# Kernel optimization log

Measured on AMD Instinct MI355X. Metric: run time of the kernel, lower is better.

## Reference

```python
import jax, jax.numpy as jnp
import numpy as np

N_LAYERS, H, D, DFF, V = 6, 16, 1024, 4096, 512
B, S = 4, 2048
DK = D // H
EPS = 1e-6
NEG = -1000000000.0


def _pe_table(max_len, d):
    pos = np.arange(max_len, dtype=np.float32)[:, None]
    div = 1.0 / (10000.0 ** (np.arange(0, d, 2, dtype=np.float32) / d))
    pe = np.zeros((max_len, d), dtype=np.float32)
    pe[:, 0::2] = np.sin(pos * div)
    pe[:, 1::2] = np.cos(pos * div)
    return jnp.asarray(pe[None])  # [1, max_len, d]


def setup_inputs() -> dict:
    key = jax.random.key(0)
    ks = jax.random.split(key, 20)
    f = lambda k, shp: (jax.random.normal(k, shp, dtype=jnp.float32) * 0.02)
    inp = {
        "tgt": jax.random.randint(ks[0], (B, S), 0, V, dtype=jnp.int64),
        "tgt_mask": jnp.tril(jnp.ones((S, S), dtype=jnp.int32))[None],  # [1,S,S] causal
        "emb": f(ks[1], (V, D)),
        "pe": _pe_table(S, D),
        "Wq": f(ks[2], (N_LAYERS, H, D, DK)), "bq": f(ks[3], (N_LAYERS, H, DK)),
        "Wk": f(ks[4], (N_LAYERS, H, D, DK)), "bk": f(ks[5], (N_LAYERS, H, DK)),
        "Wv": f(ks[6], (N_LAYERS, H, D, DK)), "bv": f(ks[7], (N_LAYERS, H, DK)),
        "Wo": f(ks[8], (N_LAYERS, D, D)), "bo": f(ks[9], (N_LAYERS, D)),
        "W1": f(ks[10], (N_LAYERS, D, DFF)), "b1": f(ks[11], (N_LAYERS, DFF)),
        "W2": f(ks[12], (N_LAYERS, DFF, D)), "b2": f(ks[13], (N_LAYERS, D)),
        "ln1_a": jnp.ones((N_LAYERS, D)), "ln1_b": jnp.zeros((N_LAYERS, D)),
        "ln2_a": jnp.ones((N_LAYERS, D)), "ln2_b": jnp.zeros((N_LAYERS, D)),
        "lnf_a": jnp.ones((D,)), "lnf_b": jnp.zeros((D,)),
    }
    return inp


def _ln(x, a, b):
    # torch: a*(x-mean)/(std+eps)+b with unbiased std
    m = x.mean(-1, keepdims=True)
    var = ((x - m) ** 2).sum(-1, keepdims=True) / (x.shape[-1] - 1)
    return a * (x - m) / (jnp.sqrt(var) + EPS) + b


def reference(tgt, tgt_mask, emb, pe, Wq, bq, Wk, bk, Wv, bv, Wo, bo,
              W1, b1, W2, b2, ln1_a, ln1_b, ln2_a, ln2_b, lnf_a, lnf_b):
    d = emb.shape[1]
    s = tgt.shape[1]
    x = emb[tgt] * jnp.sqrt(jnp.float32(d)) + pe[:, :s]  # [B,S,D]
    dk = Wq.shape[-1]
    scale = jnp.sqrt(jnp.float32(dk))

    def layer(x, p):
        wq, bq_, wk, bk_, wv, bv_, wo, bo_, w1, b1_, w2, b2_, a1, g1, a2, g2 = p
        h = _ln(x, a1, g1)
        q = jnp.einsum('bsd,hdk->bhsk', h, wq) + bq_[:, None, :]
        k = jnp.einsum('bsd,hdk->bhsk', h, wk) + bk_[:, None, :]
        v = jnp.einsum('bsd,hdk->bhsk', h, wv) + bv_[:, None, :]
        sc = jnp.einsum('bhsk,bhtk->bhst', q, k) / scale
        sc = jnp.where(tgt_mask[:, None] == 0, jnp.float32(NEG), sc)
        att = jax.nn.softmax(sc, axis=-1)
        o = jnp.einsum('bhst,bhtk->bhsk', att, v)
        o = o.transpose(0, 2, 1, 3).reshape(x.shape)  # concat heads (head order)
        x = x + (o @ wo + bo_)
        h2 = _ln(x, a2, g2)
        x = x + (jnp.maximum(h2 @ w1 + b1_, 0.0) @ w2 + b2_)
        return x, None

    x, _ = jax.lax.scan(layer, x, (Wq, bq, Wk, bk, Wv, bv, Wo, bo,
                                   W1, b1, W2, b2, ln1_a, ln1_b, ln2_a, ln2_b))
    return _ln(x, lnf_a, lnf_b)
```

## Files before the change

kernel.cpp:

```cpp
#include <hip/hip_runtime.h>

typedef __bf16 bf16;
typedef float f32x4 __attribute__((ext_vector_type(4)));
typedef __bf16 bf16x8 __attribute__((ext_vector_type(8)));
typedef __bf16 bf16x4 __attribute__((ext_vector_type(4)));
typedef __bf16 bf16x2 __attribute__((ext_vector_type(2)));

#define NL 6
#define NH 16
#define DM 1024
#define DFF 4096
#define SEQ 2048
#define NB 4
#define NTOK (NB*SEQ)

__device__ __forceinline__ void gload16(const void* g, void* l) {
  __builtin_amdgcn_global_load_lds((const __attribute__((address_space(1))) void*)g,
                                   (__attribute__((address_space(3))) void*)l, 16, 0, 0);
}

__global__ __launch_bounds__(256) void repack_t(const float* __restrict__ src,
                                                bf16* __restrict__ out, int K, int N) {
  const int l = blockIdx.z;
  const int d0 = blockIdx.x * 32, n0 = blockIdx.y * 32;
  __shared__ float t[32][33];
  const int tx = threadIdx.x & 31, ty = threadIdx.x >> 5;
  const float* s = src + (size_t)l * K * N;
  #pragma unroll
  for (int j = 0; j < 4; ++j)
    t[ty*4 + j][tx] = s[(size_t)(d0 + ty*4 + j) * N + n0 + tx];
  __syncthreads();
  bf16* o = out + (size_t)l * N * K;
  #pragma unroll
  for (int j = 0; j < 4; ++j)
    o[(size_t)(n0 + ty*4 + j) * K + d0 + tx] = (bf16)t[tx][ty*4 + j];
}

__global__ __launch_bounds__(256) void repack_qkv(const float* __restrict__ Wq,
                                                  const float* __restrict__ Wk,
                                                  const float* __restrict__ Wv,
                                                  bf16* __restrict__ out) {
  const int l = blockIdx.z;
  const int d0 = blockIdx.x * 32, n0 = blockIdx.y * 32;
  __shared__ float t[32][33];
  const int tx = threadIdx.x & 31, ty = threadIdx.x >> 5;
  const int which = n0 >> 10, h = (n0 & 1023) >> 6, kh0 = n0 & 63;
  const float* W = (which == 0) ? Wq : (which == 1 ? Wk : Wv);
  const float* s = W + ((size_t)(l*NH + h) * DM) * 64 + kh0;
  #pragma unroll
  for (int j = 0; j < 4; ++j)
    t[ty*4 + j][tx] = s[(size_t)(d0 + ty*4 + j) * 64 + tx];
  __syncthreads();
  bf16* o = out + (size_t)l * 3072 * DM + (size_t)n0 * DM + d0;
  #pragma unroll
  for (int j = 0; j < 4; ++j)
    o[(size_t)(ty*4 + j) * DM + tx] = (bf16)t[tx][ty*4 + j];
}

__global__ __launch_bounds__(256) void repack_b(const float* __restrict__ bq,
                                                const float* __restrict__ bk,
                                                const float* __restrict__ bv,
                                                float* __restrict__ out) {
  const int i = blockIdx.x * 256 + threadIdx.x;
  if (i >= NL * 3072) return;
  const int l = i / 3072, n = i % 3072;
  const int which = n >> 10, h = (n >> 6) & 15, kh = n & 63;
  const float* b = (which == 0) ? bq : (which == 1 ? bk : bv);
  out[i] = b[(l*NH + h) * 64 + kh];
}

__global__ __launch_bounds__(256) void embed_k(const int* __restrict__ tgt,
                                               const float* __restrict__ emb,
                                               const float* __restrict__ pe,
                                               float* __restrict__ x) {
  const int i = blockIdx.x;
  const int spos = i & (SEQ - 1);
  const int tok = tgt[i];
  const int tid = threadIdx.x;
  float4 e = ((const float4*)(emb + (size_t)tok * DM))[tid];
  float4 p = ((const float4*)(pe + (size_t)spos * DM))[tid];
  float4 r; r.x = e.x*32.f + p.x; r.y = e.y*32.f + p.y; r.z = e.z*32.f + p.z; r.w = e.w*32.f + p.w;
  ((float4*)(x + (size_t)i * DM))[tid] = r;
}

template<bool OB>
__global__ __launch_bounds__(256) void ln_k(const float* __restrict__ x,
                                            const float* __restrict__ a,
                                            const float* __restrict__ bsh,
                                            bf16* __restrict__ ob, float* __restrict__ of) {
  __shared__ float red[8];
  const int row = blockIdx.x, tid = threadIdx.x;
  const float4 v = ((const float4*)(x + (size_t)row * DM))[tid];
  float s = v.x + v.y + v.z + v.w;
  #pragma unroll
  for (int off = 32; off > 0; off >>= 1) s += __shfl_down(s, off);
  if ((tid & 63) == 0) red[tid >> 6] = s;
  __syncthreads();
  const float mean = (red[0] + red[1] + red[2] + red[3]) * (1.f / 1024.f);
  const float d0 = v.x - mean, d1 = v.y - mean, d2 = v.z - mean, d3 = v.w - mean;
  float ss = d0*d0 + d1*d1 + d2*d2 + d3*d3;
  #pragma unroll
  for (int off = 32; off > 0; off >>= 1) ss += __shfl_down(ss, off);
  if ((tid & 63) == 0) red[4 + (tid >> 6)] = ss;
  __syncthreads();
  const float var = (red[4] + red[5] + red[6] + red[7]) * (1.f / 1023.f);
  const float inv = 1.f / (sqrtf(var) + 1e-6f);
  const float4 av = ((const float4*)a)[tid];
  const float4 bv = ((const float4*)bsh)[tid];
  const float r0 = av.x * d0 * inv + bv.x;
  const float r1 = av.y * d1 * inv + bv.y;
  const float r2 = av.z * d2 * inv + bv.z;
  const float r3 = av.w * d3 * inv + bv.w;
  if (OB) {
    bf16x4 w; w[0] = (bf16)r0; w[1] = (bf16)r1; w[2] = (bf16)r2; w[3] = (bf16)r3;
    ((bf16x4*)(ob + (size_t)row * DM))[tid] = w;
  } else {
    float4 w; w.x = r0; w.y = r1; w.z = r2; w.w = r3;
    ((float4*)(of + (size_t)row * DM))[tid] = w;
  }
}

#define BARRIER() asm volatile("s_barrier" ::: "memory")
#define VMW(n)    asm volatile("s_waitcnt vmcnt(" #n ")" ::: "memory")

template<int EPI>
__global__ __launch_bounds__(512, 1) void gemm8(const bf16* __restrict__ A,
                                                const bf16* __restrict__ B,
                                                const float* __restrict__ bias,
                                                float* __restrict__ xres,
                                                bf16* __restrict__ outb,
                                                bf16* __restrict__ vtb,
                                                int K, int ldc) {
  constexpr bool SW = (EPI == 1) || (EPI == 2);
  __shared__ __align__(16) char lds[131072];
  const int tid = threadIdx.x;
  const int m0 = blockIdx.x * 256, n0 = blockIdx.y * 256;
  const int wid = tid >> 6, lane = tid & 63;
  const int wm = wid >> 2, wn = wid & 3;
  const int fr = lane & 15, fq = lane >> 4;
  const int fl16 = (fq * 16 + fr) * 16;
  const int s0 = tid, s1 = tid + 512;
  const int r0 = ((s0 >> 7) << 4) | (s0 & 15), c0 = (((s0 >> 6) & 1) << 2) | ((s0 >> 4) & 3);
  const int r1 = ((s1 >> 7) << 4) | (s1 & 15), c1 = (((s1 >> 6) & 1) << 2) | ((s1 >> 4) & 3);
  const bf16* Ap0 = A + (size_t)(m0 + r0) * K + c0 * 8;
  const bf16* Ap1 = A + (size_t)(m0 + r1) * K + c1 * 8;
  const bf16* Bp0 = B + (size_t)(n0 + r0) * K + c0 * 8;
  const bf16* Bp1 = B + (size_t)(n0 + r1) * K + c1 * 8;
  const size_t rskip = (size_t)128 * K;
  const int aRd = wm * 16384;
  const int bRd = 32768 + (wn >> 1) * 16384;
  const int bN = (wn & 1) * 4;

  f32x4 acc[8][4] = {};
  bf16x8 af8[8][2], bfr[4][2];

#define ST_A(d, h, kt) { \
  gload16(Ap0 + (size_t)(h) * rskip + (kt), lds + (d)*65536 + (h)*16384 + s0*16); \
  gload16(Ap1 + (size_t)(h) * rskip + (kt), lds + (d)*65536 + (h)*16384 + s1*16); }
#define ST_B(d, h, kt) { \
  gload16(Bp0 + (size_t)(h) * rskip + (kt), lds + (d)*65536 + 32768 + (h)*16384 + s0*16); \
  gload16(Bp1 + (size_t)(h) * rskip + (kt), lds + (d)*65536 + 32768 + (h)*16384 + s1*16); }
#define LD_A(d, mb) { _Pragma("unroll") for (int m_ = 0; m_ < 4; ++m_) \
    _Pragma("unroll") for (int ks_ = 0; ks_ < 2; ++ks_) \
      af8[(mb) + m_][ks_] = *(const bf16x8*)(lds + (d)*65536 + aRd + ((mb) + m_)*2048 + ks_*1024 + fl16); }
#define LD_B(d, nb) { _Pragma("unroll") for (int n_ = 0; n_ < 2; ++n_) \
    _Pragma("unroll") for (int ks_ = 0; ks_ < 2; ++ks_) \
      bfr[(nb) + n_][ks_] = *(const bf16x8*)(lds + (d)*65536 + bRd + (bN + (nb) + n_)*2048 + ks_*1024 + fl16); }
#define MFMA_Q(mb, nb) { __builtin_amdgcn_s_setprio(1); \
  _Pragma("unroll") for (int m_ = 0; m_ < 4; ++m_) \
  _Pragma("unroll") for (int n_ = 0; n_ < 2; ++n_) \
  _Pragma("unroll") for (int ks_ = 0; ks_ < 2; ++ks_) \
    acc[(mb) + m_][(nb) + n_] = SW ? \
      __builtin_amdgcn_mfma_f32_16x16x32_bf16( \
        bfr[(nb) + n_][ks_], af8[(mb) + m_][ks_], acc[(mb) + m_][(nb) + n_], 0, 0, 0) : \
      __builtin_amdgcn_mfma_f32_16x16x32_bf16( \
        af8[(mb) + m_][ks_], bfr[(nb) + n_][ks_], acc[(mb) + m_][(nb) + n_], 0, 0, 0); \
  __builtin_amdgcn_s_setprio(0); }

  ST_A(0, 0, 0); ST_A(0, 1, 0);
  ST_B(0, 0, 0); ST_B(0, 1, 0);
  ST_A(1, 0, 64); ST_A(1, 1, 64);
  VMW(4);
  BARRIER();

  const int niter = K >> 7;
  for (int it = 0; it < niter; ++it) {
    const int ktB1 = (2 * it + 1) << 6;
    const int ktE2 = (2 * it + 2) << 6;
    const int ktO3 = (2 * it + 3) << 6;
    const bool more = (it + 1 < niter);
    LD_A(0, 0); LD_B(0, 0);
    ST_B(1, 0, ktB1);
    BARRIER(); MFMA_Q(0, 0); BARRIER();
    LD_A(0, 4);
    ST_B(1, 1, ktB1);
    BARRIER(); MFMA_Q(4, 0); BARRIER();
    LD_B(0, 2);
    if (more) ST_A(0, 0, ktE2);
    BARRIER(); MFMA_Q(4, 2); BARRIER();
    if (more) { ST_A(0, 1, ktE2); VMW(4); } else { VMW(0); }
    BARRIER(); MFMA_Q(0, 2); BARRIER();
    LD_A(1, 0); LD_B(1, 0);
    if (more) ST_B(0, 0, ktE2);
    BARRIER(); MFMA_Q(0, 0); BARRIER();
    LD_A(1, 4);
    if (more) ST_B(0, 1, ktE2);
    BARRIER(); MFMA_Q(4, 0); BARRIER();
    LD_B(1, 2);
    if (more) ST_A(1, 0, ktO3);
    BARRIER(); MFMA_Q(4, 2); BARRIER();
    if (more) { ST_A(1, 1, ktO3); VMW(4); }
    BARRIER(); MFMA_Q(0, 2); BARRIER();
  }
#undef ST_A
#undef ST_B
#undef LD_A
#undef LD_B
#undef MFMA_Q

  #pragma unroll
  for (int m = 0; m < 8; ++m) {
    #pragma unroll
    for (int n = 0; n < 4; ++n) {
      if constexpr (SW) {
        const int row = m0 + wm * 128 + m * 16 + fr;
        const int colb = n0 + wn * 64 + n * 16 + fq * 4;
        const float4 b4 = *(const float4*)(bias + colb);
        if constexpr (EPI == 2) {
          bf16x4 w;
          w[0] = (bf16)fmaxf(acc[m][n][0] + b4.x, 0.f);
          w[1] = (bf16)fmaxf(acc[m][n][1] + b4.y, 0.f);
          w[2] = (bf16)fmaxf(acc[m][n][2] + b4.z, 0.f);
          w[3] = (bf16)fmaxf(acc[m][n][3] + b4.w, 0.f);
          *(bf16x4*)(outb + (size_t)row * ldc + colb) = w;
        } else {
          float4* p = (float4*)(xres + (size_t)row * ldc + colb);
          float4 c = *p;
          c.x += acc[m][n][0] + b4.x;
          c.y += acc[m][n][1] + b4.y;
          c.z += acc[m][n][2] + b4.z;
          c.w += acc[m][n][3] + b4.w;
          *p = c;
        }
      } else {
        const int row = m0 + wm * 128 + m * 16 + fq * 4;
        const int col = n0 + wn * 64 + n * 16 + fr;
        const float bc = bias[col];
        if constexpr (EPI == 3) {
          if (col >= 2048) {
            const int hh = (col - 2048) >> 6, dkk = col & 63;
            const int bb = row >> 11, tt = row & 2047;
            bf16x4 w;
            #pragma unroll
            for (int jj = 0; jj < 4; ++jj) w[jj] = (bf16)(acc[m][n][jj] + bc);
            *(bf16x4*)(vtb + ((((size_t)bb*NH + hh)*64 + dkk)*SEQ + tt)) = w;
            continue;
          }
        }
        #pragma unroll
        for (int j = 0; j < 4; ++j) {
          float v = acc[m][n][j] + bc;
          if constexpr (EPI == 3) {
            if (col < 1024) v *= 0.125f;
          }
          outb[(size_t)(row + j) * ldc + col] = (bf16)v;
        }
      }
    }
  }
}

template<int EPI>
__global__ __launch_bounds__(512, 1) void gemm8n(const bf16* __restrict__ A,
                                                 const bf16* __restrict__ B,
                                                 const float* __restrict__ bias,
                                                 float* __restrict__ xres,
                                                 bf16* __restrict__ outb,
                                                 bf16* __restrict__ vtb,
                                                 int K, int ldc) {
  constexpr bool SW = (EPI == 1) || (EPI == 2);
  __shared__ __align__(16) char lds[131072];
  const int tid = threadIdx.x;
  const int m0 = blockIdx.x * 128, n0 = blockIdx.y * 256;
  const int wid = tid >> 6, lane = tid & 63;
  const int wm = wid >> 2, wn = wid & 3;
  const int fr = lane & 15, fq = lane >> 4;
  const int fl16 = (fq * 16 + fr) * 16;
  const int s0 = tid, s1 = tid + 512;
  const int r0 = ((s0 >> 7) << 4) | (s0 & 15), c0 = (((s0 >> 6) & 1) << 2) | ((s0 >> 4) & 3);
  const int r1 = ((s1 >> 7) << 4) | (s1 & 15), c1 = (((s1 >> 6) & 1) << 2) | ((s1 >> 4) & 3);
  const bf16* Ap0 = A + (size_t)(m0 + r0) * K + c0 * 8;
  const bf16* Ap1 = A + (size_t)(m0 + r1) * K + c1 * 8;
  const bf16* Bp0 = B + (size_t)(n0 + r0) * K + c0 * 8;
  const bf16* Bp1 = B + (size_t)(n0 + r1) * K + c1 * 8;
  const size_t rskipB = (size_t)128 * K;
  const int aRd = wm * 8192;
  const int bRd = wn * 8192;

  f32x4 acc[4][4] = {};
  bf16x8 af[4][2], bfr[4][2];

#define ST_An(d, kt) { \
  gload16(Ap0 + (kt), lds + (d)*16384 + s0*16); \
  gload16(Ap1 + (kt), lds + (d)*16384 + s1*16); }
#define ST_Bn(j, h, kt) { \
  gload16(Bp0 + (size_t)(h) * rskipB + (kt), lds + 32768 + (j)*32768 + (h)*16384 + s0*16); \
  gload16(Bp1 + (size_t)(h) * rskipB + (kt), lds + 32768 + (j)*32768 + (h)*16384 + s1*16); }
#define LD_An(d) { _Pragma("unroll") for (int m_ = 0; m_ < 4; ++m_) \
    _Pragma("unroll") for (int ks_ = 0; ks_ < 2; ++ks_) \
      af[m_][ks_] = *(const bf16x8*)(lds + (d)*16384 + aRd + m_*2048 + ks_*1024 + fl16); }
#define LD_Bn(j, nb) { _Pragma("unroll") for (int n_ = 0; n_ < 2; ++n_) \
    _Pragma("unroll") for (int ks_ = 0; ks_ < 2; ++ks_) \
      bfr[(nb) + n_][ks_] = *(const bf16x8*)(lds + 32768 + (j)*32768 + bRd + ((nb) + n_)*2048 + ks_*1024 + fl16); }
#define MFMA_H(nb) { __builtin_amdgcn_s_setprio(1); \
  _Pragma("unroll") for (int m_ = 0; m_ < 4; ++m_) \
  _Pragma("unroll") for (int n_ = 0; n_ < 2; ++n_) \
  _Pragma("unroll") for (int ks_ = 0; ks_ < 2; ++ks_) \
    acc[m_][(nb) + n_] = SW ? \
      __builtin_amdgcn_mfma_f32_16x16x32_bf16( \
        bfr[(nb) + n_][ks_], af[m_][ks_], acc[m_][(nb) + n_], 0, 0, 0) : \
      __builtin_amdgcn_mfma_f32_16x16x32_bf16( \
        af[m_][ks_], bfr[(nb) + n_][ks_], acc[m_][(nb) + n_], 0, 0, 0); \
  __builtin_amdgcn_s_setprio(0); }

  ST_An(0, 0);
  ST_Bn(0, 0, 0); ST_Bn(0, 1, 0);
  ST_An(1, 64);
  ST_Bn(1, 0, 64); ST_Bn(1, 1, 64);
  VMW(0);
  BARRIER();

  const int nt = K >> 6;
  int j = 0;
  for (int t = 0; t < nt; ++t) {
    const int d = t & 1;
    const int j2 = (j + 2 >= 3) ? (j - 1) : (j + 2);
    const bool more = (t + 2 < nt);
    const int kt2 = (t + 2) << 6;
    LD_An(d); LD_Bn(j, 0);
    if (more) { ST_Bn(j2, 0, kt2); ST_Bn(j2, 1, kt2); }
    BARRIER(); MFMA_H(0); BARRIER();
    LD_Bn(j, 2);
    if (more) { ST_An(d, kt2); VMW(6); } else { VMW(0); }
    BARRIER(); MFMA_H(2); BARRIER();
    j = (j + 1 >= 3) ? 0 : (j + 1);
  }
#undef ST_An
#undef ST_Bn
#undef LD_An
#undef LD_Bn
#undef MFMA_H

  #pragma unroll
  for (int m = 0; m < 4; ++m) {
    #pragma unroll
    for (int n = 0; n < 4; ++n) {
      if constexpr (SW) {
        const int row = m0 + wm * 64 + m * 16 + fr;
        const int colb = n0 + wn * 64 + n * 16 + fq * 4;
        const float4 b4 = *(const float4*)(bias + colb);
        if constexpr (EPI == 2) {
          bf16x4 w;
          w[0] = (bf16)fmaxf(acc[m][n][0] + b4.x, 0.f);
          w[1] = (bf16)fmaxf(acc[m][n][1] + b4.y, 0.f);
          w[2] = (bf16)fmaxf(acc[m][n][2] + b4.z, 0.f);
          w[3] = (bf16)fmaxf(acc[m][n][3] + b4.w, 0.f);
          *(bf16x4*)(outb + (size_t)row * ldc + colb) = w;
        } else {
          float4* p = (float4*)(xres + (size_t)row * ldc + colb);
          float4 c = *p;
          c.x += acc[m][n][0] + b4.x;
          c.y += acc[m][n][1] + b4.y;
          c.z += acc[m][n][2] + b4.z;
          c.w += acc[m][n][3] + b4.w;
          *p = c;
        }
      } else {
        const int row = m0 + wm * 64 + m * 16 + fq * 4;
        const int col = n0 + wn * 64 + n * 16 + fr;
        const float bc = bias[col];
        if constexpr (EPI == 3) {
          if (col >= 2048) {
            const int hh = (col - 2048) >> 6, dkk = col & 63;
            const int bb = row >> 11, tt = row & 2047;
            bf16x4 w;
            #pragma unroll
            for (int jj = 0; jj < 4; ++jj) w[jj] = (bf16)(acc[m][n][jj] + bc);
            *(bf16x4*)(vtb + ((((size_t)bb*NH + hh)*64 + dkk)*SEQ + tt)) = w;
            continue;
          }
        }
        #pragma unroll
        for (int jj = 0; jj < 4; ++jj) {
          float v = acc[m][n][jj] + bc;
          if constexpr (EPI == 3) {
            if (col < 1024) v *= 0.125f;
          }
          outb[(size_t)(row + jj) * ldc + col] = (bf16)v;
        }
      }
    }
  }
}

__global__ __launch_bounds__(256) void attn5_k(const bf16* __restrict__ qk,
                                               const bf16* __restrict__ vt,
                                               bf16* __restrict__ o) {
  __shared__ __align__(16) bf16 Ks[2][64 * 64];
  __shared__ __align__(16) bf16 Vs[2][64 * 64];
  __shared__ __align__(16) bf16 Ps[4][16 * 64];
  const int flat = blockIdx.y * 16 + blockIdx.x;
  const int xcd = flat & 7, slot = flat >> 3;
  const int bh = xcd * 8 + (slot >> 4);
  const int pairi = slot & 15;
  const int b = bh >> 4, h = bh & 15;
  const int tid = threadIdx.x;
  const int wave = tid >> 6, lane = tid & 63;
  const int fr = lane & 15, fq = lane >> 4;
  const bf16* Qg = qk + (size_t)b * SEQ * 2048 + h * 64;
  const bf16* Kg = Qg + 1024;
  const bf16* Vtg = vt + (size_t)bh * 64 * SEQ;
  char* Pw = (char*)&Ps[wave][0];
  const int fr7 = fr & 7;

  const int sl0 = tid, sl1 = tid + 256;
  const int sr0 = sl0 >> 3, sm0 = sl0 & 7, sg0 = (sm0 ^ (sr0 & 7)) * 8;
  const int sr1 = sl1 >> 3, sm1 = sl1 & 7, sg1 = (sm1 ^ (sr1 & 7)) * 8;

#define STAGE_KV(db, t0_) { \
    gload16(Kg + (size_t)((t0_) + sr0) * 2048 + sg0, (char*)Ks + (db)*8192 + sl0*16); \
    gload16(Vtg + (size_t)sr0 * SEQ + (t0_) + sg0,   (char*)Vs + (db)*8192 + sl0*16); \
    gload16(Kg + (size_t)((t0_) + sr1) * 2048 + sg1, (char*)Ks + (db)*8192 + sl1*16); \
    gload16(Vtg + (size_t)sr1 * SEQ + (t0_) + sg1,   (char*)Vs + (db)*8192 + sl1*16); }

#define COMPUTE(q0w_, qrow_, qf0_, qf1_, oacc_, lrun_) { \
      f32x4 s_[4] = {}; \
      __builtin_amdgcn_s_setprio(1); \
      _Pragma("unroll") \
      for (int n = 0; n < 4; ++n) { \
        const int t_ = n * 16 + fr; \
        const bf16x8 k0 = *(const bf16x8*)(Ksc + (t_ * 8 + (fq ^ (t_ & 7))) * 16); \
        const bf16x8 k1 = *(const bf16x8*)(Ksc + (t_ * 8 + ((fq + 4) ^ (t_ & 7))) * 16); \
        s_[n] = __builtin_amdgcn_mfma_f32_16x16x32_bf16(k0, (qf0_), s_[n], 0, 0, 0); \
        s_[n] = __builtin_amdgcn_mfma_f32_16x16x32_bf16(k1, (qf1_), s_[n], 0, 0, 0); \
      } \
      __builtin_amdgcn_s_setprio(0); \
      float sv[16]; \
      _Pragma("unroll") \
      for (int n = 0; n < 4; ++n) \
        _Pragma("unroll") \
        for (int jj = 0; jj < 4; ++jj) \
          sv[n * 4 + jj] = s_[n][jj]; \
      if (t0 + 63 > (q0w_)) { \
        _Pragma("unroll") \
        for (int i = 0; i < 16; ++i) { \
          const int t_abs = t0 + (i >> 2) * 16 + fq * 4 + (i & 3); \
          if (t_abs > (qrow_)) sv[i] = -1e30f; \
        } \
      } \
      _Pragma("unroll") \
      for (int i = 0; i < 16; ++i) sv[i] = __expf(sv[i]); \
      float a8[8]; \
      _Pragma("unroll") \
      for (int i = 0; i < 8; ++i) a8[i] = sv[i] + sv[i + 8]; \
      float a4[4]; \
      _Pragma("unroll") \
      for (int i = 0; i < 4; ++i) a4[i] = a8[i] + a8[i + 4]; \
      float ps = (a4[0] + a4[1]) + (a4[2] + a4[3]); \
      ps += __shfl_xor(ps, 16); \
      ps += __shfl_xor(ps, 32); \
      (lrun_) += ps; \
      _Pragma("unroll") \
      for (int n = 0; n < 4; ++n) \
        _Pragma("unroll") \
        for (int jp = 0; jp < 2; ++jp) { \
          bf16x2 w; w[0] = (bf16)sv[n * 4 + jp * 2]; w[1] = (bf16)sv[n * 4 + jp * 2 + 1]; \
          const int byteoff = n * 32 + fq * 8 + jp * 4; \
          const int chunk = byteoff >> 4, within = byteoff & 15; \
          *(bf16x2*)(Pw + fr * 128 + ((chunk ^ fr7) << 4) + within) = w; \
        } \
      __builtin_amdgcn_s_setprio(1); \
      _Pragma("unroll") \
      for (int ks = 0; ks < 2; ++ks) { \
        const bf16x8 pa = *(const bf16x8*)(Pw + fr * 128 + (((ks * 4 + fq) ^ fr7) << 4)); \
        _Pragma("unroll") \
        for (int nd = 0; nd < 4; ++nd) { \
          const int dk_ = nd * 16 + fr; \
          const bf16x8 vf = *(const bf16x8*)(Vsc + (dk_ * 8 + ((ks * 4 + fq) ^ (dk_ & 7))) * 16); \
          (oacc_)[nd] = __builtin_amdgcn_mfma_f32_16x16x32_bf16(pa, vf, (oacc_)[nd], 0, 0, 0); \
        } \
      } \
      __builtin_amdgcn_s_setprio(0); }

  const int qbA = pairi;
  const int qbB = 31 - pairi;
  const int q0A = qbA * 64 + wave * 16, q0B = qbB * 64 + wave * 16;
  const int qrA = q0A + fr, qrB = q0B + fr;
  const bf16x8 qA0 = *(const bf16x8*)(Qg + (size_t)qrA * 2048 + fq * 8);
  const bf16x8 qA1 = *(const bf16x8*)(Qg + (size_t)qrA * 2048 + 32 + fq * 8);
  const bf16x8 qB0 = *(const bf16x8*)(Qg + (size_t)qrB * 2048 + fq * 8);
  const bf16x8 qB1 = *(const bf16x8*)(Qg + (size_t)qrB * 2048 + 32 + fq * 8);
  f32x4 oaccA[4] = {}, oaccB[4] = {};
  float lA = 0.f, lB = 0.f;
  const int nt = qbB + 1;

  STAGE_KV(0, 0);
  for (int kt = 0; kt < nt; ++kt) {
    const int t0 = kt * 64;
    const int db = kt & 1;
    __syncthreads();
    if (kt + 1 < nt) {
      STAGE_KV(db ^ 1, (kt + 1) * 64);
      VMW(4);
    } else {
      VMW(0);
    }
    __syncthreads();
    const char* Ksc = (char*)Ks + db * 8192;
    const char* Vsc = (char*)Vs + db * 8192;
    if (t0 <= q0A + 15) COMPUTE(q0A, qrA, qA0, qA1, oaccA, lA);
    COMPUTE(q0B, qrB, qB0, qB1, oaccB, lB);
  }
#undef COMPUTE
#undef STAGE_KV

  {
    float li[4];
    #pragma unroll
    for (int jj = 0; jj < 4; ++jj) li[jj] = 1.f / __shfl(lA, fq * 4 + jj);
    #pragma unroll
    for (int nd = 0; nd < 4; ++nd) {
      const int col = h * 64 + nd * 16 + fr;
      #pragma unroll
      for (int jj = 0; jj < 4; ++jj) {
        const int row = q0A + fq * 4 + jj;
        o[((size_t)b * SEQ + row) * DM + col] = (bf16)(oaccA[nd][jj] * li[jj]);
      }
    }
    #pragma unroll
    for (int jj = 0; jj < 4; ++jj) li[jj] = 1.f / __shfl(lB, fq * 4 + jj);
    #pragma unroll
    for (int nd = 0; nd < 4; ++nd) {
      const int col = h * 64 + nd * 16 + fr;
      #pragma unroll
      for (int jj = 0; jj < 4; ++jj) {
        const int row = q0B + fq * 4 + jj;
        o[((size_t)b * SEQ + row) * DM + col] = (bf16)(oaccB[nd][jj] * li[jj]);
      }
    }
  }
}

extern "C" void kernel_launch(void* const* d_in, const int* in_sizes, int n_in,
                              void* d_out, int out_size, void* d_ws, size_t ws_size,
                              hipStream_t stream) {
  const int*   tgt  = (const int*)d_in[0];
  const float* emb  = (const float*)d_in[2];
  const float* pe   = (const float*)d_in[3];
  const float* Wq   = (const float*)d_in[4];
  const float* bq   = (const float*)d_in[5];
  const float* Wk   = (const float*)d_in[6];
  const float* bk   = (const float*)d_in[7];
  const float* Wv   = (const float*)d_in[8];
  const float* bv   = (const float*)d_in[9];
  const float* Wo   = (const float*)d_in[10];
  const float* bo   = (const float*)d_in[11];
  const float* W1   = (const float*)d_in[12];
  const float* b1   = (const float*)d_in[13];
  const float* W2   = (const float*)d_in[14];
  const float* b2   = (const float*)d_in[15];
  const float* ln1a = (const float*)d_in[16];
  const float* ln1b = (const float*)d_in[17];
  const float* ln2a = (const float*)d_in[18];
  const float* ln2b = (const float*)d_in[19];
  const float* lnfa = (const float*)d_in[20];
  const float* lnfb = (const float*)d_in[21];

  char* ws = (char*)d_ws;
  size_t off = 0;
  bf16*  wqkv = (bf16*)(ws + off);  off += (size_t)NL * 3072 * DM * 2;
  bf16*  wo_  = (bf16*)(ws + off);  off += (size_t)NL * DM * DM * 2;
  bf16*  w1_  = (bf16*)(ws + off);  off += (size_t)NL * DFF * DM * 2;
  bf16*  w2_  = (bf16*)(ws + off);  off += (size_t)NL * DM * DFF * 2;
  float* bqkv = (float*)(ws + off); off += (size_t)NL * 3072 * 4;
  float* x    = (float*)(ws + off); off += (size_t)NTOK * DM * 4;
  bf16*  hbuf = (bf16*)(ws + off);  off += (size_t)NTOK * DM * 2;
  bf16*  qkb  = (bf16*)(ws + off);  off += (size_t)NTOK * 2048 * 2;
  bf16*  vtb  = (bf16*)(ws + off);  off += (size_t)NB * NH * 64 * SEQ * 2;
  bf16*  obuf = (bf16*)(ws + off);  off += (size_t)NTOK * DM * 2;
  bf16*  ubuf = qkb;

  repack_qkv<<<dim3(32, 96, NL), 256, 0, stream>>>(Wq, Wk, Wv, wqkv);
  repack_t  <<<dim3(32, 32, NL), 256, 0, stream>>>(Wo, wo_, DM, DM);
  repack_t  <<<dim3(32, 128, NL), 256, 0, stream>>>(W1, w1_, DM, DFF);
  repack_t  <<<dim3(128, 32, NL), 256, 0, stream>>>(W2, w2_, DFF, DM);
  repack_b  <<<72, 256, 0, stream>>>(bq, bk, bv, bqkv);
  embed_k   <<<NTOK, 256, 0, stream>>>(tgt, emb, pe, x);

  for (int l = 0; l < NL; ++l) {
    ln_k<true><<<NTOK, 256, 0, stream>>>(x, ln1a + l * DM, ln1b + l * DM, hbuf, nullptr);
    gemm8<3><<<dim3(32, 12), 512, 0, stream>>>(hbuf, wqkv + (size_t)l * 3072 * DM,
                                               bqkv + l * 3072, nullptr, qkb, vtb, DM, 2048);
    attn5_k<<<dim3(16, 64), 256, 0, stream>>>(qkb, vtb, obuf);
    gemm8n<1><<<dim3(64, 4), 512, 0, stream>>>(obuf, wo_ + (size_t)l * DM * DM,
                                               bo + l * DM, x, nullptr, nullptr, DM, DM);
    ln_k<true><<<NTOK, 256, 0, stream>>>(x, ln2a + l * DM, ln2b + l * DM, hbuf, nullptr);
    gemm8<2><<<dim3(32, 16), 512, 0, stream>>>(hbuf, w1_ + (size_t)l * DFF * DM,
                                               b1 + l * DFF, nullptr, ubuf, nullptr, DM, DFF);
    gemm8n<1><<<dim3(64, 4), 512, 0, stream>>>(ubuf, w2_ + (size_t)l * DM * DFF,
                                               b2 + l * DM, x, nullptr, nullptr, DFF, DM);
  }
  ln_k<false><<<NTOK, 256, 0, stream>>>(x, lnfa, lnfb, nullptr, (float*)d_out);

  (void)in_sizes; (void)n_in; (void)out_size; (void)ws_size;
}
```

Before: 2.548 ms.

## Widen attention KV tiles to 128 keys and fold Q scaling into weights

The attention kernel now stages 128-key K/V tiles per iteration instead of 64, which halves the loop trip count and the block-wide barriers, and does more MFMA work per synchronisation. LDS use doubles to about 72KB, which may lower occupancy, and register pressure rises from the larger score arrays. Separately, the 1/8 query scaling moves into the one-time weight and bias repack, removing a per-element multiply from the QKV GEMM epilogue. The rounding of the scaled Q changes slightly because the weights are scaled before conversion to bf16.

```diff
diff --git a/kernel.cpp b/kernel.cpp
--- a/kernel.cpp
+++ b/kernel.cpp
@@ -46,6 +46,7 @@
   const int tx = threadIdx.x & 31, ty = threadIdx.x >> 5;
   const int which = n0 >> 10, h = (n0 & 1023) >> 6, kh0 = n0 & 63;
   const float* W = (which == 0) ? Wq : (which == 1 ? Wk : Wv);
+  const float qs = (which == 0) ? 0.125f : 1.f;
   const float* s = W + ((size_t)(l*NH + h) * DM) * 64 + kh0;
   #pragma unroll
   for (int j = 0; j < 4; ++j)
@@ -54,7 +55,7 @@
   bf16* o = out + (size_t)l * 3072 * DM + (size_t)n0 * DM + d0;
   #pragma unroll
   for (int j = 0; j < 4; ++j)
-    o[(size_t)(ty*4 + j) * DM + tx] = (bf16)t[tx][ty*4 + j];
+    o[(size_t)(ty*4 + j) * DM + tx] = (bf16)(t[tx][ty*4 + j] * qs);
 }
 
 __global__ __launch_bounds__(256) void repack_b(const float* __restrict__ bq,
@@ -66,7 +67,7 @@
   const int l = i / 3072, n = i % 3072;
   const int which = n >> 10, h = (n >> 6) & 15, kh = n & 63;
   const float* b = (which == 0) ? bq : (which == 1 ? bk : bv);
-  out[i] = b[(l*NH + h) * 64 + kh];
+  out[i] = b[(l*NH + h) * 64 + kh] * ((which == 0) ? 0.125f : 1.f);
 }
 
 __global__ __launch_bounds__(256) void embed_k(const int* __restrict__ tgt,
@@ -259,10 +260,7 @@
         }
         #pragma unroll
         for (int j = 0; j < 4; ++j) {
-          float v = acc[m][n][j] + bc;
-          if constexpr (EPI == 3) {
-            if (col < 1024) v *= 0.125f;
-          }
+          const float v = acc[m][n][j] + bc;
           outb[(size_t)(row + j) * ldc + col] = (bf16)v;
         }
       }
@@ -392,10 +390,7 @@
         }
         #pragma unroll
         for (int jj = 0; jj < 4; ++jj) {
-          float v = acc[m][n][jj] + bc;
-          if constexpr (EPI == 3) {
-            if (col < 1024) v *= 0.125f;
-          }
+          const float v = acc[m][n][jj] + bc;
           outb[(size_t)(row + jj) * ldc + col] = (bf16)v;
         }
       }
@@ -406,9 +401,9 @@
 __global__ __launch_bounds__(256) void attn5_k(const bf16* __restrict__ qk,
                                                const bf16* __restrict__ vt,
                                                bf16* __restrict__ o) {
-  __shared__ __align__(16) bf16 Ks[2][64 * 64];
-  __shared__ __align__(16) bf16 Vs[2][64 * 64];
-  __shared__ __align__(16) bf16 Ps[4][16 * 64];
+  __shared__ __align__(16) bf16 Ks[2][128 * 64];
+  __shared__ __align__(16) bf16 Vs[2][64 * 128];
+  __shared__ __align__(16) bf16 Ps[4][16 * 128];
   const int flat = blockIdx.y * 16 + blockIdx.x;
   const int xcd = flat & 7, slot = flat >> 3;
   const int bh = xcd * 8 + (slot >> 4);
@@ -423,21 +418,18 @@
   char* Pw = (char*)&Ps[wave][0];
   const int fr7 = fr & 7;
 
-  const int sl0 = tid, sl1 = tid + 256;
-  const int sr0 = sl0 >> 3, sm0 = sl0 & 7, sg0 = (sm0 ^ (sr0 & 7)) * 8;
-  const int sr1 = sl1 >> 3, sm1 = sl1 & 7, sg1 = (sm1 ^ (sr1 & 7)) * 8;
-
-#define STAGE_KV(db, t0_) { \
-    gload16(Kg + (size_t)((t0_) + sr0) * 2048 + sg0, (char*)Ks + (db)*8192 + sl0*16); \
-    gload16(Vtg + (size_t)sr0 * SEQ + (t0_) + sg0,   (char*)Vs + (db)*8192 + sl0*16); \
-    gload16(Kg + (size_t)((t0_) + sr1) * 2048 + sg1, (char*)Ks + (db)*8192 + sl1*16); \
-    gload16(Vtg + (size_t)sr1 * SEQ + (t0_) + sg1,   (char*)Vs + (db)*8192 + sl1*16); }
+#define STAGE_KV(db, t0_) { _Pragma("unroll") for (int s2 = 0; s2 < 4; ++s2) { \
+    const int sl = tid + s2 * 256; \
+    const int kr = sl >> 3, kmm = sl & 7, kgc = (kmm ^ (kr & 7)) * 8; \
+    gload16(Kg + (size_t)((t0_) + kr) * 2048 + kgc, (char*)Ks + (db)*16384 + sl*16); \
+    const int vr = sl >> 4, vmm = sl & 15, vgc = (vmm ^ (vr & 7)) * 8; \
+    gload16(Vtg + (size_t)vr * SEQ + (t0_) + vgc, (char*)Vs + (db)*16384 + sl*16); } }
 
 #define COMPUTE(q0w_, qrow_, qf0_, qf1_, oacc_, lrun_) { \
-      f32x4 s_[4] = {}; \
+      f32x4 s_[8] = {}; \
       __builtin_amdgcn_s_setprio(1); \
       _Pragma("unroll") \
-      for (int n = 0; n < 4; ++n) { \
+      for (int n = 0; n < 8; ++n) { \
         const int t_ = n * 16 + fr; \
         const bf16x8 k0 = *(const bf16x8*)(Ksc + (t_ * 8 + (fq ^ (t_ & 7))) * 16); \
         const bf16x8 k1 = *(const bf16x8*)(Ksc + (t_ * 8 + ((fq + 4) ^ (t_ & 7))) * 16); \
@@ -445,24 +437,27 @@
         s_[n] = __builtin_amdgcn_mfma_f32_16x16x32_bf16(k1, (qf1_), s_[n], 0, 0, 0); \
       } \
       __builtin_amdgcn_s_setprio(0); \
-      float sv[16]; \
-      _Pragma("unroll") \
-      for (int n = 0; n < 4; ++n) \
+      float sv[32]; \
+      _Pragma("unroll") \
+      for (int n = 0; n < 8; ++n) \
         _Pragma("unroll") \
         for (int jj = 0; jj < 4; ++jj) \
           sv[n * 4 + jj] = s_[n][jj]; \
-      if (t0 + 63 > (q0w_)) { \
+      if (t0 + 127 > (q0w_)) { \
         _Pragma("unroll") \
-        for (int i = 0; i < 16; ++i) { \
+        for (int i = 0; i < 32; ++i) { \
           const int t_abs = t0 + (i >> 2) * 16 + fq * 4 + (i & 3); \
           if (t_abs > (qrow_)) sv[i] = -1e30f; \
         } \
       } \
       _Pragma("unroll") \
-      for (int i = 0; i < 16; ++i) sv[i] = __expf(sv[i]); \
+      for (int i = 0; i < 32; ++i) sv[i] = __expf(sv[i]); \
+      float a16[16]; \
+      _Pragma("unroll") \
+      for (int i = 0; i < 16; ++i) a16[i] = sv[i] + sv[i + 16]; \
       float a8[8]; \
       _Pragma("unroll") \
-      for (int i = 0; i < 8; ++i) a8[i] = sv[i] + sv[i + 8]; \
+      for (int i = 0; i < 8; ++i) a8[i] = a16[i] + a16[i + 8]; \
       float a4[4]; \
       _Pragma("unroll") \
       for (int i = 0; i < 4; ++i) a4[i] = a8[i] + a8[i + 4]; \
@@ -471,22 +466,22 @@
       ps += __shfl_xor(ps, 32); \
       (lrun_) += ps; \
       _Pragma("unroll") \
-      for (int n = 0; n < 4; ++n) \
+      for (int n = 0; n < 8; ++n) \
         _Pragma("unroll") \
         for (int jp = 0; jp < 2; ++jp) { \
           bf16x2 w; w[0] = (bf16)sv[n * 4 + jp * 2]; w[1] = (bf16)sv[n * 4 + jp * 2 + 1]; \
           const int byteoff = n * 32 + fq * 8 + jp * 4; \
           const int chunk = byteoff >> 4, within = byteoff & 15; \
-          *(bf16x2*)(Pw + fr * 128 + ((chunk ^ fr7) << 4) + within) = w; \
+          *(bf16x2*)(Pw + fr * 256 + ((chunk ^ fr7) << 4) + within) = w; \
         } \
       __builtin_amdgcn_s_setprio(1); \
       _Pragma("unroll") \
-      for (int ks = 0; ks < 2; ++ks) { \
-        const bf16x8 pa = *(const bf16x8*)(Pw + fr * 128 + (((ks * 4 + fq) ^ fr7) << 4)); \
+      for (int ks = 0; ks < 4; ++ks) { \
+        const bf16x8 pa = *(const bf16x8*)(Pw + fr * 256 + (((ks * 4 + fq) ^ fr7) << 4)); \
         _Pragma("unroll") \
         for (int nd = 0; nd < 4; ++nd) { \
           const int dk_ = nd * 16 + fr; \
-          const bf16x8 vf = *(const bf16x8*)(Vsc + (dk_ * 8 + ((ks * 4 + fq) ^ (dk_ & 7))) * 16); \
+          const bf16x8 vf = *(const bf16x8*)(Vsc + (dk_ * 16 + ((ks * 4 + fq) ^ (dk_ & 7))) * 16); \
           (oacc_)[nd] = __builtin_amdgcn_mfma_f32_16x16x32_bf16(pa, vf, (oacc_)[nd], 0, 0, 0); \
         } \
       } \
@@ -502,22 +497,22 @@
   const bf16x8 qB1 = *(const bf16x8*)(Qg + (size_t)qrB * 2048 + 32 + fq * 8);
   f32x4 oaccA[4] = {}, oaccB[4] = {};
   float lA = 0.f, lB = 0.f;
-  const int nt = qbB + 1;
+  const int nt = (qbB * 64 + 63) / 128 + 1;
 
   STAGE_KV(0, 0);
   for (int kt = 0; kt < nt; ++kt) {
-    const int t0 = kt * 64;
+    const int t0 = kt * 128;
     const int db = kt & 1;
     __syncthreads();
     if (kt + 1 < nt) {
-      STAGE_KV(db ^ 1, (kt + 1) * 64);
-      VMW(4);
+      STAGE_KV(db ^ 1, (kt + 1) * 128);
+      VMW(8);
     } else {
       VMW(0);
     }
     __syncthreads();
-    const char* Ksc = (char*)Ks + db * 8192;
-    const char* Vsc = (char*)Vs + db * 8192;
+    const char* Ksc = (char*)Ks + db * 16384;
+    const char* Vsc = (char*)Vs + db * 16384;
     if (t0 <= q0A + 15) COMPUTE(q0A, qrA, qA0, qA1, oaccA, lA);
     COMPUTE(q0B, qrB, qB0, qB1, oaccB, lB);
   }
```

Result: no change. 2.525 ms (-0.9%).
